# Kernel tuning notes

Hardware: AMD Instinct MI355X
Metric: run time of the kernel (lower is better)

The kernel has to match this reference:

```python
import jax, jax.numpy as jnp
import numpy as np

B, LQ, LS, S = 64, 64, 512, 512
NEG = -1e6


def mask_for_lengths(lengths, max_len, mask_right=True):
    pos = jnp.arange(max_len)
    if mask_right:
        m = pos[None, :] >= lengths[:, None]
    else:
        m = pos[None, :] < lengths[:, None]
    return jnp.where(m, jnp.float32(NEG), jnp.float32(0.0))


def setup_inputs() -> dict:
    key = jax.random.key(0)
    ks = jax.random.split(key, 12)
    f = lambda k, shp: jax.random.normal(k, shp, jnp.float32)
    sc = np.float32(1.0 / np.sqrt(S))
    return {
        "encoded_question": f(ks[0], (B, LQ, S)),
        "encoded_support": f(ks[1], (B, LS, S)),
        "question_length": jax.random.randint(ks[2], (B,), 1, LQ + 1),
        "support_length": jax.random.randint(ks[3], (B,), LS // 2, LS + 1),
        "correct_start": jax.random.randint(ks[4], (B,), 0, LS),
        "answer2question": jnp.arange(B),
        "is_eval": 1,
        "W_qa": f(ks[5], (S, 1)) * sc,
        "W_qsi": f(ks[6], (S, S)) * sc,
        "b_qsi": jnp.zeros((S,), jnp.float32),
        "W_qs": f(ks[7], (2 * S, S)) * sc,
        "W_ss": f(ks[8], (S, 1)) * sc,
        "W_qei": f(ks[9], (S, S)) * sc,
        "b_qei": jnp.zeros((S,), jnp.float32),
        "W_qe": f(ks[10], (3 * S, S)) * sc,
        "W_es": f(ks[11], (S, 1)) * sc,
    }


def reference(encoded_question, encoded_support, question_length, support_length,
              correct_start, answer2question, is_eval,
              W_qa, W_qsi, b_qsi, W_qs, W_ss, W_qei, b_qei, W_qe, W_es):
    # question attention pooling
    att = jnp.einsum('bqd,do->bq', encoded_question, W_qa)
    att = att + mask_for_lengths(question_length, LQ)
    w = jax.nn.softmax(att, axis=1)                                   # [B,LQ]
    q_state = jnp.einsum('bqd,bq->bd', encoded_question, w)           # [B,S]

    # start scoring
    start_input = jnp.concatenate(
        [q_state[:, None, :] * encoded_support, encoded_support], axis=2)  # [B,LS,2S]
    q_start_inter = q_state @ W_qsi + b_qsi                           # [B,S]
    q_start_state = start_input @ W_qs + q_start_inter[:, None, :]    # [B,LS,S]
    support_mask = mask_for_lengths(support_length, LS)
    start_scores = jnp.einsum('bld,do->bl', jax.nn.relu(q_start_state), W_ss)
    start_scores = start_scores + support_mask                        # [B,LS]
    predicted_start_pointer = jnp.argmax(start_scores, axis=1)        # [B]

    # eval path: start_pointer = predicted argmax
    start_pointer = predicted_start_pointer
    u_s = jnp.take_along_axis(encoded_support,
                              start_pointer[:, None, None], axis=1)[:, 0, :]  # [B,S]

    # end scoring
    end_input = jnp.concatenate(
        [encoded_support * u_s[:, None, :], start_input], axis=2)     # [B,LS,3S]
    q_end_inter = q_state @ W_qei + b_qei
    q_end_state = end_input @ W_qe + q_end_inter[:, None, :]          # [B,LS,S]
    end_scores = jnp.einsum('bld,do->bl', jax.nn.relu(q_end_state), W_es)
    end_scores = end_scores + support_mask
    # eval: mask positions left of start_pointer
    end_scores = end_scores + mask_for_lengths(start_pointer, LS, mask_right=False)
    predicted_end_pointer = jnp.argmax(end_scores, axis=1)

    return (start_scores, end_scores, predicted_start_pointer, predicted_end_pointer)
```

## Files before the change

### kernel.cpp

```cpp
#include <hip/hip_runtime.h>
#include <math.h>

constexpr int B_  = 64;
constexpr int LQ_ = 64;
constexpr int LS_ = 512;
constexpr int S_  = 512;
#define NEGV (-1e6f)
#define MARGIN 0.0625f

typedef __attribute__((ext_vector_type(8))) short bf16x8;
typedef __attribute__((ext_vector_type(4))) float f32x4;

__device__ inline unsigned short f2bf_rn(float x) {
    unsigned u = __builtin_bit_cast(unsigned, x);
    unsigned r = (u + 0x7FFFu + ((u >> 16) & 1u)) >> 16;
    return (unsigned short)r;
}

__global__ __launch_bounds__(512)
void prep_support_kernel(const float* __restrict__ support, short* __restrict__ Aprep)
{
    int bid = blockIdx.x;
    int b = bid >> 3, rg = bid & 7;
    int t = threadIdx.x;
    int r  = t & 63;
    int cg = t >> 6;
    int row  = rg * 64 + r;
    int rc   = row >> 8;
    int rowp = row & 255;
    const float* src = support + ((size_t)(b * LS_ + row)) * S_;

    #pragma unroll
    for (int ii = 0; ii < 2; ++ii) {
        int i = cg * 2 + ii;
        #pragma unroll
        for (int kc = 0; kc < 4; ++kc) {
            int d0 = i * 32 + kc * 8;
            float4 f0 = *(const float4*)(src + d0);
            float4 f1 = *(const float4*)(src + d0 + 4);
            uint4 H;
            H.x = f2bf_rn(f0.x) | ((unsigned)f2bf_rn(f0.y) << 16);
            H.y = f2bf_rn(f0.z) | ((unsigned)f2bf_rn(f0.w) << 16);
            H.z = f2bf_rn(f1.x) | ((unsigned)f2bf_rn(f1.y) << 16);
            H.w = f2bf_rn(f1.z) | ((unsigned)f2bf_rn(f1.w) << 16);
            size_t off = ((size_t)(b * 2 + rc) * 16 + i) * 8192 + kc * 2048 + rowp * 8;
            *(uint4*)&Aprep[off] = H;
        }
    }
}

__global__ __launch_bounds__(256)
void qpool_kernel(const float* __restrict__ eq, const int* __restrict__ qlen,
                  const float* __restrict__ W_qa, float* __restrict__ q_state)
{
    int b = blockIdx.x;
    int t = threadIdx.x;
    int wave = t >> 6, lane = t & 63;
    __shared__ float att[LQ_];
    __shared__ float wsm[LQ_];
    const float* eqb = eq + (size_t)b * LQ_ * S_;

    for (int k = 0; k < 16; ++k) {
        int q = wave + 4 * k;
        const float* row = eqb + q * S_;
        float s = 0.f;
        #pragma unroll
        for (int j = 0; j < S_ / 64; ++j)
            s = fmaf(row[lane + 64 * j], W_qa[lane + 64 * j], s);
        #pragma unroll
        for (int off = 32; off >= 1; off >>= 1)
            s += __shfl_xor(s, off);
        if (lane == 0) att[q] = s;
    }
    __syncthreads();

    if (wave == 0) {
        int L = qlen[b];
        float v = att[lane] + ((lane < L) ? 0.f : NEGV);
        float m = v;
        #pragma unroll
        for (int off = 32; off >= 1; off >>= 1)
            m = fmaxf(m, __shfl_xor(m, off));
        float e = expf(v - m);
        float sum = e;
        #pragma unroll
        for (int off = 32; off >= 1; off >>= 1)
            sum += __shfl_xor(sum, off);
        wsm[lane] = e / sum;
    }
    __syncthreads();

    for (int d = t; d < S_; d += 256) {
        float acc = 0.f;
        #pragma unroll 8
        for (int q = 0; q < LQ_; ++q)
            acc = fmaf(wsm[q], eqb[q * S_ + d], acc);
        q_state[b * S_ + d] = acc;
    }
}

__global__ __launch_bounds__(512)
void inter_kernel(const float* __restrict__ q_state,
                  const float* __restrict__ W_qsi, const float* __restrict__ b_qsi,
                  const float* __restrict__ W_qei, const float* __restrict__ b_qei,
                  float* __restrict__ qsi, float* __restrict__ qei)
{
    int b = blockIdx.x;
    const float* W  = blockIdx.y ? W_qei : W_qsi;
    const float* bi = blockIdx.y ? b_qei : b_qsi;
    float*       o  = blockIdx.y ? qei   : qsi;
    int t = threadIdx.x, lane = t & 63, w = t >> 6;
    __shared__ float qs[S_];
    __shared__ float red[8][S_];
    qs[t] = q_state[b * S_ + t];
    __syncthreads();

    float z[8];
    #pragma unroll
    for (int k = 0; k < 8; ++k) z[k] = 0.f;
    const int d0 = w * 64;
    #pragma unroll 4
    for (int dd = 0; dd < 64; ++dd) {
        int d = d0 + dd;
        float q = qs[d];
        const float* row = W + (size_t)d * S_ + lane;
        #pragma unroll
        for (int k = 0; k < 8; ++k)
            z[k] = fmaf(q, row[k * 64], z[k]);
    }
    #pragma unroll
    for (int k = 0; k < 8; ++k) red[w][k * 64 + lane] = z[k];
    __syncthreads();
    float acc = bi[t];
    #pragma unroll
    for (int ww = 0; ww < 8; ++ww) acc += red[ww][t];
    o[b * S_ + t] = acc;
}

template <int NT>
__global__ __launch_bounds__(512)
void prep_kernel(const float* __restrict__ W, const float* __restrict__ q_state,
                 const float* __restrict__ u_s, short* __restrict__ Wc)
{
    int bid = blockIdx.x;
    int i = bid >> 6, b = bid & 63;
    int col = threadIdx.x;
    int cc = col >> 8, colp = col & 255;
    __shared__ float scq[32], scu[32];
    if (col < 32) scq[col] = q_state[b * S_ + i * 32 + col];
    if (NT == 3 && col >= 32 && col < 64) scu[col - 32] = u_s[b * S_ + i * 32 + col - 32];
    __syncthreads();

    unsigned short h[32];
    #pragma unroll
    for (int d = 0; d < 32; ++d) {
        int D = i * 32 + d;
        float v;
        if (NT == 2)
            v = fmaf(scq[d], W[(size_t)D * S_ + col], W[(size_t)(S_ + D) * S_ + col]);
        else
            v = fmaf(scu[d], W[(size_t)D * S_ + col],
                fmaf(scq[d], W[(size_t)(S_ + D) * S_ + col], W[(size_t)(2 * S_ + D) * S_ + col]));
        h[d] = f2bf_rn(v);
    }
    size_t base = ((size_t)(b * 2 + cc) * 16 + i) * 8192 + (size_t)colp * 8;
    #pragma unroll
    for (int kc = 0; kc < 4; ++kc) {
        uint4 H;
        H.x = h[kc*8+0] | ((unsigned)h[kc*8+1] << 16);
        H.y = h[kc*8+2] | ((unsigned)h[kc*8+3] << 16);
        H.z = h[kc*8+4] | ((unsigned)h[kc*8+5] << 16);
        H.w = h[kc*8+6] | ((unsigned)h[kc*8+7] << 16);
        *(uint4*)&Wc[base + kc * 2048] = H;
    }
}

__global__ __launch_bounds__(512, 2)
void score_kernel(const short* __restrict__ Aprep, const short* __restrict__ Wc,
                  const float* __restrict__ inter, const float* __restrict__ Wsmall,
                  float* __restrict__ out)
{
    const int t = threadIdx.x;
    const int lane = t & 63, wid = t >> 6;
    const int wr = wid >> 2, wc = wid & 3;
    const int l15 = lane & 15, l4 = lane >> 4;

    int lid = blockIdx.x;
    int xcd = lid & 7, slot = lid >> 3;
    int b  = xcd * 8 + (slot >> 2);
    int rc = (slot >> 1) & 1;
    int cc = slot & 1;

    __shared__ __attribute__((aligned(16))) short As[2][8192];
    __shared__ __attribute__((aligned(16))) short Bs[2][8192];
    __shared__ float int_l[256], wsm_l[256];
    __shared__ float sm_red[256][4];

    if (t < 256) {
        int_l[t] = inter[b * S_ + cc * 256 + t];
        wsm_l[t] = Wsmall[cc * 256 + t];
    }

    const char* Abase = (const char*)(Aprep + ((size_t)(b * 2 + rc) * 16) * 8192);
    const char* Bbase = (const char*)(Wc    + ((size_t)(b * 2 + cc) * 16) * 8192);

    f32x4 acc[8][4];
    #pragma unroll
    for (int r = 0; r < 8; ++r)
        #pragma unroll
        for (int c = 0; c < 4; ++c)
            acc[r][c] = (f32x4){0.f, 0.f, 0.f, 0.f};

    auto stage = [&](int i, int buf) {
        const char* ga = Abase + (size_t)i * 16384 + t * 16;
        const char* gb = Bbase + (size_t)i * 16384 + t * 16;
        char* la = (char*)As[buf] + t * 16;
        char* lb = (char*)Bs[buf] + t * 16;
        __builtin_amdgcn_global_load_lds(
            (const __attribute__((address_space(1))) void*)ga,
            (__attribute__((address_space(3))) void*)la, 16, 0, 0);
        __builtin_amdgcn_global_load_lds(
            (const __attribute__((address_space(1))) void*)(ga + 8192),
            (__attribute__((address_space(3))) void*)(la + 8192), 16, 0, 0);
        __builtin_amdgcn_global_load_lds(
            (const __attribute__((address_space(1))) void*)gb,
            (__attribute__((address_space(3))) void*)lb, 16, 0, 0);
        __builtin_amdgcn_global_load_lds(
            (const __attribute__((address_space(1))) void*)(gb + 8192),
            (__attribute__((address_space(3))) void*)(lb + 8192), 16, 0, 0);
    };

    stage(0, 0);

    for (int i = 0; i < 16; ++i) {
        const int buf = i & 1;
        if (i + 1 < 16) {
            stage(i + 1, buf ^ 1);
            asm volatile("s_waitcnt vmcnt(4)" ::: "memory");
        } else {
            asm volatile("s_waitcnt vmcnt(0)" ::: "memory");
        }
        __builtin_amdgcn_s_barrier();

        bf16x8 ah[8];
        #pragma unroll
        for (int r = 0; r < 8; ++r) {
            int rowp = wr * 128 + r * 16 + l15;
            ah[r] = *(const bf16x8*)&As[buf][l4 * 2048 + rowp * 8];
        }
        #pragma unroll
        for (int c = 0; c < 4; ++c) {
            int colp = wc * 64 + c * 16 + l15;
            bf16x8 bh = *(const bf16x8*)&Bs[buf][l4 * 2048 + colp * 8];
            #pragma unroll
            for (int r = 0; r < 8; ++r)
                acc[r][c] = __builtin_amdgcn_mfma_f32_16x16x32_bf16(ah[r], bh, acc[r][c], 0, 0, 0);
        }
        asm volatile("s_waitcnt lgkmcnt(0)" ::: "memory");
        __builtin_amdgcn_s_barrier();
    }

    #pragma unroll
    for (int r = 0; r < 8; ++r) {
        #pragma unroll
        for (int jj = 0; jj < 4; ++jj) {
            float pr = 0.f;
            #pragma unroll
            for (int c = 0; c < 4; ++c) {
                int colp = wc * 64 + c * 16 + l15;
                float v = acc[r][c][jj] + int_l[colp];
                v = fmaxf(v, 0.f);
                pr = fmaf(v, wsm_l[colp], pr);
            }
            pr += __shfl_xor(pr, 1);
            pr += __shfl_xor(pr, 2);
            pr += __shfl_xor(pr, 4);
            pr += __shfl_xor(pr, 8);
            if (l15 == 0) sm_red[wr * 128 + r * 16 + l4 * 4 + jj][wc] = pr;
        }
    }
    __syncthreads();
    if (t < 256) {
        int l = rc * 256 + t;
        float s = sm_red[t][0] + sm_red[t][1] + sm_red[t][2] + sm_red[t][3];
        out[((size_t)cc * B_ * LS_) + b * LS_ + l] = s;
    }
}

__global__ __launch_bounds__(256)
void combine_kernel(const float* __restrict__ part0, const float* __restrict__ part1,
                    const int* __restrict__ slen, const int* __restrict__ sp,
                    int endflag, float* __restrict__ out)
{
    int g = blockIdx.x * 256 + threadIdx.x;
    int b = g >> 9, l = g & 511;
    float s = part0[g] + part1[g];
    if (l >= slen[b]) s += NEGV;
    if (endflag && l < sp[b]) s += NEGV;
    out[g] = s;
}

__device__ inline int select_cands(const float* s_l, int t, int lane, int w,
                                   float* wred, int* wcnt, int* cand)
{
    float v = s_l[t];
    #pragma unroll
    for (int off = 32; off >= 1; off >>= 1)
        v = fmaxf(v, __shfl_xor(v, off));
    if (lane == 0) wred[w] = v;
    __syncthreads();
    float m = wred[0];
    #pragma unroll
    for (int k = 1; k < 8; ++k) m = fmaxf(m, wred[k]);
    float th = m - MARGIN;
    bool flag = s_l[t] >= th;
    unsigned long long bal = __ballot(flag);
    int rank = __popcll(bal & ((1ull << lane) - 1ull));
    if (lane == 0) wcnt[w] = (int)__popcll(bal);
    __syncthreads();
    int off = 0, total = 0;
    #pragma unroll
    for (int k = 0; k < 8; ++k) { if (k < w) off += wcnt[k]; total += wcnt[k]; }
    if (flag) { int pos = off + rank; if (pos < 8) cand[pos] = t; }
    __syncthreads();
    return total < 8 ? total : 8;
}

template <bool END>
__global__ __launch_bounds__(512)
void rescue_kernel(const float* __restrict__ support, const float* __restrict__ q_state,
                   const float* __restrict__ u_s, const float* __restrict__ Wbig,
                   const float* __restrict__ inter, const float* __restrict__ Wsmall,
                   const float* __restrict__ scores, float* __restrict__ part)
{
    int bid = blockIdx.x;
    int b = bid >> 2, chunk = bid & 3;
    int t = threadIdx.x, lane = t & 63, w = t >> 6;
    __shared__ float s_l[S_], qs_l[S_], us_l[S_];
    __shared__ float arow[8][S_];
    __shared__ float red[8][8][128];
    __shared__ float wred[8];
    __shared__ int wcnt[8], cand[8];

    s_l[t]  = scores[b * S_ + t];
    qs_l[t] = q_state[b * S_ + t];
    if (END) us_l[t] = u_s[b * S_ + t];
    #pragma unroll
    for (int c = 0; c < 8; ++c) arow[c][t] = 0.f;
    __syncthreads();

    int cnt = select_cands(s_l, t, lane, w, wred, wcnt, cand);

    for (int c = 0; c < cnt; ++c)
        arow[c][t] = support[((size_t)(b * LS_ + cand[c])) * S_ + t];
    __syncthreads();

    float z0[8], z1[8];
    #pragma unroll
    for (int c = 0; c < 8; ++c) { z0[c] = 0.f; z1[c] = 0.f; }

    const int d0 = w * 64;
    const int s0 = chunk * 128 + lane, s1 = s0 + 64;
    const float* W1 = Wbig;
    const float* W2 = Wbig + (size_t)S_ * S_;
    const float* W3 = Wbig + (size_t)2 * S_ * S_;

    #pragma unroll 4
    for (int dd = 0; dd < 64; ++dd) {
        int d = d0 + dd;
        float r1a = W1[(size_t)d * S_ + s0], r1b = W1[(size_t)d * S_ + s1];
        float r2a = W2[(size_t)d * S_ + s0], r2b = W2[(size_t)d * S_ + s1];
        float r3a = 0.f, r3b = 0.f;
        if (END) { r3a = W3[(size_t)d * S_ + s0]; r3b = W3[(size_t)d * S_ + s1]; }
        float q = qs_l[d];
        float u = END ? us_l[d] : 0.f;
        #pragma unroll
        for (int c = 0; c < 8; ++c) {
            float a = arow[c][d];
            if (END) {
                float ua = u * a, qa = q * a;
                z0[c] = fmaf(ua, r1a, fmaf(qa, r2a, fmaf(a, r3a, z0[c])));
                z1[c] = fmaf(ua, r1b, fmaf(qa, r2b, fmaf(a, r3b, z1[c])));
            } else {
                float qa = q * a;
                z0[c] = fmaf(qa, r1a, fmaf(a, r2a, z0[c]));
                z1[c] = fmaf(qa, r1b, fmaf(a, r2b, z1[c]));
            }
        }
    }
    #pragma unroll
    for (int c = 0; c < 8; ++c) {
        red[w][c][lane]      = z0[c];
        red[w][c][64 + lane] = z1[c];
    }
    __syncthreads();

    {
        float a0 = 0.f, a1 = 0.f;
        #pragma unroll
        for (int ww = 0; ww < 8; ++ww) {
            a0 += red[ww][w][lane];
            a1 += red[ww][w][64 + lane];
        }
        float v0 = fmaxf(a0 + inter[b * S_ + s0], 0.f) * Wsmall[s0];
        float v1 = fmaxf(a1 + inter[b * S_ + s1], 0.f) * Wsmall[s1];
        float p = v0 + v1;
        #pragma unroll
        for (int off = 32; off >= 1; off >>= 1)
            p += __shfl_xor(p, off);
        if (lane == 0 && w < cnt) part[((size_t)b * 8 + w) * 4 + chunk] = p;
    }
}

template <bool END>
__global__ __launch_bounds__(512)
void finalize_kernel(const float* __restrict__ scores, const float* __restrict__ part,
                     const float* __restrict__ support, int* __restrict__ sp_ws,
                     float* __restrict__ pred, float* __restrict__ us_out)
{
    int b = blockIdx.x;
    int t = threadIdx.x, lane = t & 63, w = t >> 6;
    __shared__ float s_l[S_];
    __shared__ float wred[8];
    __shared__ int wcnt[8], cand[8];
    __shared__ int best_sh;

    s_l[t] = scores[b * S_ + t];
    __syncthreads();
    int cnt = select_cands(s_l, t, lane, w, wred, wcnt, cand);

    if (t == 0) {
        float bv = -INFINITY;
        int bi = cand[0];
        for (int c = 0; c < cnt; ++c) {
            const float* pp = part + ((size_t)b * 8 + c) * 4;
            float e = ((pp[0] + pp[1]) + pp[2]) + pp[3];
            if (e > bv) { bv = e; bi = cand[c]; }
        }
        best_sh = bi;
        pred[b] = (float)bi;
        if (!END) sp_ws[b] = bi;
    }
    __syncthreads();
    if (!END)
        us_out[b * S_ + t] = support[((size_t)(b * LS_ + best_sh)) * S_ + t];
}

extern "C" void kernel_launch(void* const* d_in, const int* in_sizes, int n_in,
                              void* d_out, int out_size, void* d_ws, size_t ws_size,
                              hipStream_t stream)
{
    const float* eq    = (const float*)d_in[0];
    const float* es    = (const float*)d_in[1];
    const int*   qlen  = (const int*)d_in[2];
    const int*   slen  = (const int*)d_in[3];
    const float* W_qa  = (const float*)d_in[7];
    const float* W_qsi = (const float*)d_in[8];
    const float* b_qsi = (const float*)d_in[9];
    const float* W_qs  = (const float*)d_in[10];
    const float* W_ss  = (const float*)d_in[11];
    const float* W_qei = (const float*)d_in[12];
    const float* b_qei = (const float*)d_in[13];
    const float* W_qe  = (const float*)d_in[14];
    const float* W_es  = (const float*)d_in[15];

    float* out          = (float*)d_out;
    float* start_scores = out;
    float* end_scores   = out + B_ * LS_;
    float* pred_start   = out + 2 * B_ * LS_;
    float* pred_end     = out + 2 * B_ * LS_ + B_;

    float* ws      = (float*)d_ws;
    float* q_state = ws;
    float* qsi     = ws + B_ * S_;
    float* qei     = ws + 2 * B_ * S_;
    float* u_s     = ws + 3 * B_ * S_;
    float* part    = ws + 4 * B_ * S_;
    int*   sp_ws   = (int*)(ws + 4 * B_ * S_ + 2048);
    float* scpart  = ws + 4 * B_ * S_ + 4096;
    short* Wc      = (short*)(scpart + 2 * B_ * LS_);
    short* Aprep   = Wc + (size_t)B_ * 2 * 16 * 8192;

    prep_support_kernel<<<512, 512, 0, stream>>>(es, Aprep);
    qpool_kernel<<<B_, 256, 0, stream>>>(eq, qlen, W_qa, q_state);
    inter_kernel<<<dim3(B_, 2), 512, 0, stream>>>(q_state, W_qsi, b_qsi, W_qei, b_qei, qsi, qei);

    prep_kernel<2><<<1024, 512, 0, stream>>>(W_qs, q_state, nullptr, Wc);
    score_kernel<<<256, 512, 0, stream>>>(Aprep, Wc, qsi, W_ss, scpart);
    combine_kernel<<<B_ * LS_ / 256, 256, 0, stream>>>(scpart, scpart + B_ * LS_,
                                                       slen, sp_ws, 0, start_scores);
    rescue_kernel<false><<<256, 512, 0, stream>>>(es, q_state, nullptr, W_qs, qsi, W_ss,
                                                  start_scores, part);
    finalize_kernel<false><<<B_, 512, 0, stream>>>(start_scores, part, es, sp_ws, pred_start, u_s);

    prep_kernel<3><<<1024, 512, 0, stream>>>(W_qe, q_state, u_s, Wc);
    score_kernel<<<256, 512, 0, stream>>>(Aprep, Wc, qei, W_es, scpart);
    combine_kernel<<<B_ * LS_ / 256, 256, 0, stream>>>(scpart, scpart + B_ * LS_,
                                                       slen, sp_ws, 1, end_scores);
    rescue_kernel<true><<<256, 512, 0, stream>>>(es, q_state, u_s, W_qe, qei, W_es,
                                                 end_scores, part);
    finalize_kernel<true><<<B_, 512, 0, stream>>>(end_scores, part, es, nullptr, pred_end, nullptr);
}
```

Measured before the change: 190.4 us.

## Retile score GEMM to full columns, fuse combine and rescue-finalize kernels

```diff
diff --git a/kernel.cpp b/kernel.cpp
--- a/kernel.cpp
+++ b/kernel.cpp
@@ -26,7 +26,7 @@
     int r  = t & 63;
     int cg = t >> 6;
     int row  = rg * 64 + r;
-    int rc   = row >> 8;
+    int rc2  = row >> 8;
     int rowp = row & 255;
     const float* src = support + ((size_t)(b * LS_ + row)) * S_;
 
@@ -43,7 +43,7 @@
             H.y = f2bf_rn(f0.z) | ((unsigned)f2bf_rn(f0.w) << 16);
             H.z = f2bf_rn(f1.x) | ((unsigned)f2bf_rn(f1.y) << 16);
             H.w = f2bf_rn(f1.z) | ((unsigned)f2bf_rn(f1.w) << 16);
-            size_t off = ((size_t)(b * 2 + rc) * 16 + i) * 8192 + kc * 2048 + rowp * 8;
+            size_t off = ((size_t)(b * 2 + rc2) * 16 + i) * 8192 + kc * 2048 + rowp * 8;
             *(uint4*)&Aprep[off] = H;
         }
     }
@@ -145,7 +145,6 @@
     int bid = blockIdx.x;
     int i = bid >> 6, b = bid & 63;
     int col = threadIdx.x;
-    int cc = col >> 8, colp = col & 255;
     __shared__ float scq[32], scu[32];
     if (col < 32) scq[col] = q_state[b * S_ + i * 32 + col];
     if (NT == 3 && col >= 32 && col < 64) scu[col - 32] = u_s[b * S_ + i * 32 + col - 32];
@@ -163,7 +162,7 @@
                 fmaf(scq[d], W[(size_t)(S_ + D) * S_ + col], W[(size_t)(2 * S_ + D) * S_ + col]));
         h[d] = f2bf_rn(v);
     }
-    size_t base = ((size_t)(b * 2 + cc) * 16 + i) * 8192 + (size_t)colp * 8;
+    size_t base = ((size_t)b * 16 + i) * 16384 + (size_t)col * 8;
     #pragma unroll
     for (int kc = 0; kc < 4; ++kc) {
         uint4 H;
@@ -171,13 +170,15 @@
         H.y = h[kc*8+2] | ((unsigned)h[kc*8+3] << 16);
         H.z = h[kc*8+4] | ((unsigned)h[kc*8+5] << 16);
         H.w = h[kc*8+6] | ((unsigned)h[kc*8+7] << 16);
-        *(uint4*)&Wc[base + kc * 2048] = H;
-    }
-}
-
+        *(uint4*)&Wc[base + kc * 4096] = H;
+    }
+}
+
+template <bool END>
 __global__ __launch_bounds__(512, 2)
 void score_kernel(const short* __restrict__ Aprep, const short* __restrict__ Wc,
                   const float* __restrict__ inter, const float* __restrict__ Wsmall,
+                  const int* __restrict__ slen, const int* __restrict__ sp,
                   float* __restrict__ out)
 {
     const int t = threadIdx.x;
@@ -188,46 +189,42 @@
     int lid = blockIdx.x;
     int xcd = lid & 7, slot = lid >> 3;
     int b  = xcd * 8 + (slot >> 2);
-    int rc = (slot >> 1) & 1;
-    int cc = slot & 1;
-
-    __shared__ __attribute__((aligned(16))) short As[2][8192];
-    __shared__ __attribute__((aligned(16))) short Bs[2][8192];
-    __shared__ float int_l[256], wsm_l[256];
-    __shared__ float sm_red[256][4];
-
-    if (t < 256) {
-        int_l[t] = inter[b * S_ + cc * 256 + t];
-        wsm_l[t] = Wsmall[cc * 256 + t];
-    }
-
-    const char* Abase = (const char*)(Aprep + ((size_t)(b * 2 + rc) * 16) * 8192);
-    const char* Bbase = (const char*)(Wc    + ((size_t)(b * 2 + cc) * 16) * 8192);
-
-    f32x4 acc[8][4];
-    #pragma unroll
-    for (int r = 0; r < 8; ++r)
-        #pragma unroll
-        for (int c = 0; c < 4; ++c)
+    int rc = slot & 3;
+    int rc2 = rc >> 1, hh = rc & 1;
+
+    __shared__ __attribute__((aligned(16))) short As[2][4096];
+    __shared__ __attribute__((aligned(16))) short Bs[2][16384];
+    __shared__ float int_l[S_], wsm_l[S_];
+    __shared__ float sm_red[128][4];
+
+    int_l[t] = inter[b * S_ + t];
+    wsm_l[t] = Wsmall[t];
+
+    const char* Abase = (const char*)(Aprep + ((size_t)(b * 2 + rc2) * 16) * 8192);
+    const char* Bbase = (const char*)(Wc    + ((size_t)b * 16) * 16384);
+
+    f32x4 acc[4][8];
+    #pragma unroll
+    for (int r = 0; r < 4; ++r)
+        #pragma unroll
+        for (int c = 0; c < 8; ++c)
             acc[r][c] = (f32x4){0.f, 0.f, 0.f, 0.f};
 
+    const int akc = t >> 7, ar = t & 127;
+
     auto stage = [&](int i, int buf) {
-        const char* ga = Abase + (size_t)i * 16384 + t * 16;
-        const char* gb = Bbase + (size_t)i * 16384 + t * 16;
+        const char* ga = Abase + (size_t)i * 16384 + akc * 4096 + hh * 2048 + ar * 16;
         char* la = (char*)As[buf] + t * 16;
-        char* lb = (char*)Bs[buf] + t * 16;
         __builtin_amdgcn_global_load_lds(
             (const __attribute__((address_space(1))) void*)ga,
             (__attribute__((address_space(3))) void*)la, 16, 0, 0);
-        __builtin_amdgcn_global_load_lds(
-            (const __attribute__((address_space(1))) void*)(ga + 8192),
-            (__attribute__((address_space(3))) void*)(la + 8192), 16, 0, 0);
-        __builtin_amdgcn_global_load_lds(
-            (const __attribute__((address_space(1))) void*)gb,
-            (__attribute__((address_space(3))) void*)lb, 16, 0, 0);
-        __builtin_amdgcn_global_load_lds(
-            (const __attribute__((address_space(1))) void*)(gb + 8192),
-            (__attribute__((address_space(3))) void*)(lb + 8192), 16, 0, 0);
+        const char* gb = Bbase + (size_t)i * 32768 + t * 16;
+        char* lb = (char*)Bs[buf] + t * 16;
+        #pragma unroll
+        for (int q = 0; q < 4; ++q)
+            __builtin_amdgcn_global_load_lds(
+                (const __attribute__((address_space(1))) void*)(gb + q * 8192),
+                (__attribute__((address_space(3))) void*)(lb + q * 8192), 16, 0, 0);
     };
 
     stage(0, 0);
@@ -236,24 +233,24 @@
         const int buf = i & 1;
         if (i + 1 < 16) {
             stage(i + 1, buf ^ 1);
-            asm volatile("s_waitcnt vmcnt(4)" ::: "memory");
+            asm volatile("s_waitcnt vmcnt(5)" ::: "memory");
         } else {
             asm volatile("s_waitcnt vmcnt(0)" ::: "memory");
         }
         __builtin_amdgcn_s_barrier();
 
-        bf16x8 ah[8];
-        #pragma unroll
-        for (int r = 0; r < 8; ++r) {
-            int rowp = wr * 128 + r * 16 + l15;
-            ah[r] = *(const bf16x8*)&As[buf][l4 * 2048 + rowp * 8];
-        }
-        #pragma unroll
-        for (int c = 0; c < 4; ++c) {
-            int colp = wc * 64 + c * 16 + l15;
-            bf16x8 bh = *(const bf16x8*)&Bs[buf][l4 * 2048 + colp * 8];
-            #pragma unroll
-            for (int r = 0; r < 8; ++r)
+        bf16x8 ah[4];
+        #pragma unroll
+        for (int r = 0; r < 4; ++r) {
+            int rowp = wr * 64 + r * 16 + l15;
+            ah[r] = *(const bf16x8*)&As[buf][l4 * 1024 + rowp * 8];
+        }
+        #pragma unroll
+        for (int c = 0; c < 8; ++c) {
+            int col = wc * 128 + c * 16 + l15;
+            bf16x8 bh = *(const bf16x8*)&Bs[buf][l4 * 4096 + col * 8];
+            #pragma unroll
+            for (int r = 0; r < 4; ++r)
                 acc[r][c] = __builtin_amdgcn_mfma_f32_16x16x32_bf16(ah[r], bh, acc[r][c], 0, 0, 0);
         }
         asm volatile("s_waitcnt lgkmcnt(0)" ::: "memory");
@@ -261,43 +258,32 @@
     }
 
     #pragma unroll
-    for (int r = 0; r < 8; ++r) {
+    for (int r = 0; r < 4; ++r) {
         #pragma unroll
         for (int jj = 0; jj < 4; ++jj) {
             float pr = 0.f;
             #pragma unroll
-            for (int c = 0; c < 4; ++c) {
-                int colp = wc * 64 + c * 16 + l15;
-                float v = acc[r][c][jj] + int_l[colp];
+            for (int c = 0; c < 8; ++c) {
+                int col = wc * 128 + c * 16 + l15;
+                float v = acc[r][c][jj] + int_l[col];
                 v = fmaxf(v, 0.f);
-                pr = fmaf(v, wsm_l[colp], pr);
+                pr = fmaf(v, wsm_l[col], pr);
             }
             pr += __shfl_xor(pr, 1);
             pr += __shfl_xor(pr, 2);
             pr += __shfl_xor(pr, 4);
             pr += __shfl_xor(pr, 8);
-            if (l15 == 0) sm_red[wr * 128 + r * 16 + l4 * 4 + jj][wc] = pr;
-        }
-    }
-    __syncthreads();
-    if (t < 256) {
-        int l = rc * 256 + t;
+            if (l15 == 0) sm_red[wr * 64 + r * 16 + l4 * 4 + jj][wc] = pr;
+        }
+    }
+    __syncthreads();
+    if (t < 128) {
+        int l = rc * 128 + t;
         float s = sm_red[t][0] + sm_red[t][1] + sm_red[t][2] + sm_red[t][3];
-        out[((size_t)cc * B_ * LS_) + b * LS_ + l] = s;
-    }
-}
-
-__global__ __launch_bounds__(256)
-void combine_kernel(const float* __restrict__ part0, const float* __restrict__ part1,
-                    const int* __restrict__ slen, const int* __restrict__ sp,
-                    int endflag, float* __restrict__ out)
-{
-    int g = blockIdx.x * 256 + threadIdx.x;
-    int b = g >> 9, l = g & 511;
-    float s = part0[g] + part1[g];
-    if (l >= slen[b]) s += NEGV;
-    if (endflag && l < sp[b]) s += NEGV;
-    out[g] = s;
+        if (l >= slen[b]) s += NEGV;
+        if (END) { if (l < sp[b]) s += NEGV; }
+        out[b * LS_ + l] = s;
+    }
 }
 
 __device__ inline int select_cands(const float* s_l, int t, int lane, int w,
@@ -328,23 +314,28 @@
 
 template <bool END>
 __global__ __launch_bounds__(512)
-void rescue_kernel(const float* __restrict__ support, const float* __restrict__ q_state,
-                   const float* __restrict__ u_s, const float* __restrict__ Wbig,
-                   const float* __restrict__ inter, const float* __restrict__ Wsmall,
-                   const float* __restrict__ scores, float* __restrict__ part)
-{
-    int bid = blockIdx.x;
-    int b = bid >> 2, chunk = bid & 3;
+void rescue_fin_kernel(const float* __restrict__ support, const float* __restrict__ q_state,
+                       const float* __restrict__ u_s_in, const float* __restrict__ Wbig,
+                       const float* __restrict__ inter, const float* __restrict__ Wsmall,
+                       const float* __restrict__ scores,
+                       int* __restrict__ sp_ws, float* __restrict__ pred,
+                       float* __restrict__ us_out)
+{
+    int b = blockIdx.x;
     int t = threadIdx.x, lane = t & 63, w = t >> 6;
-    __shared__ float s_l[S_], qs_l[S_], us_l[S_];
+    __shared__ float s_l[S_], qs_l[S_], us_l[S_], int_l[S_], wsm_l[S_];
     __shared__ float arow[8][S_];
-    __shared__ float red[8][8][128];
+    __shared__ float red[8][4][S_];
     __shared__ float wred[8];
     __shared__ int wcnt[8], cand[8];
-
-    s_l[t]  = scores[b * S_ + t];
-    qs_l[t] = q_state[b * S_ + t];
-    if (END) us_l[t] = u_s[b * S_ + t];
+    __shared__ float exact_v[8];
+    __shared__ int best_sh;
+
+    s_l[t]   = scores[b * S_ + t];
+    qs_l[t]  = q_state[b * S_ + t];
+    int_l[t] = inter[b * S_ + t];
+    wsm_l[t] = Wsmall[t];
+    if (END) us_l[t] = u_s_in[b * S_ + t];
     #pragma unroll
     for (int c = 0; c < 8; ++c) arow[c][t] = 0.f;
     __syncthreads();
@@ -355,86 +346,78 @@
         arow[c][t] = support[((size_t)(b * LS_ + cand[c])) * S_ + t];
     __syncthreads();
 
-    float z0[8], z1[8];
-    #pragma unroll
-    for (int c = 0; c < 8; ++c) { z0[c] = 0.f; z1[c] = 0.f; }
-
-    const int d0 = w * 64;
-    const int s0 = chunk * 128 + lane, s1 = s0 + 64;
     const float* W1 = Wbig;
     const float* W2 = Wbig + (size_t)S_ * S_;
     const float* W3 = Wbig + (size_t)2 * S_ * S_;
-
-    #pragma unroll 4
-    for (int dd = 0; dd < 64; ++dd) {
-        int d = d0 + dd;
-        float r1a = W1[(size_t)d * S_ + s0], r1b = W1[(size_t)d * S_ + s1];
-        float r2a = W2[(size_t)d * S_ + s0], r2b = W2[(size_t)d * S_ + s1];
-        float r3a = 0.f, r3b = 0.f;
-        if (END) { r3a = W3[(size_t)d * S_ + s0]; r3b = W3[(size_t)d * S_ + s1]; }
-        float q = qs_l[d];
-        float u = END ? us_l[d] : 0.f;
-        #pragma unroll
-        for (int c = 0; c < 8; ++c) {
-            float a = arow[c][d];
-            if (END) {
-                float ua = u * a, qa = q * a;
-                z0[c] = fmaf(ua, r1a, fmaf(qa, r2a, fmaf(a, r3a, z0[c])));
-                z1[c] = fmaf(ua, r1b, fmaf(qa, r2b, fmaf(a, r3b, z1[c])));
-            } else {
-                float qa = q * a;
-                z0[c] = fmaf(qa, r1a, fmaf(a, r2a, z0[c]));
-                z1[c] = fmaf(qa, r1b, fmaf(a, r2b, z1[c]));
+    const int d0 = w * 64;
+
+    for (int g = 0; g * 4 < cnt; ++g) {
+        float z[4][8];
+        #pragma unroll
+        for (int cc = 0; cc < 4; ++cc)
+            #pragma unroll
+            for (int j = 0; j < 8; ++j) z[cc][j] = 0.f;
+
+        #pragma unroll 2
+        for (int dd = 0; dd < 64; ++dd) {
+            int d = d0 + dd;
+            float q = qs_l[d];
+            float u = END ? us_l[d] : 0.f;
+            float a[4], qa[4], ua[4];
+            #pragma unroll
+            for (int cc = 0; cc < 4; ++cc) {
+                a[cc]  = arow[g * 4 + cc][d];
+                qa[cc] = q * a[cc];
+                if (END) ua[cc] = u * a[cc];
             }
-        }
-    }
-    #pragma unroll
-    for (int c = 0; c < 8; ++c) {
-        red[w][c][lane]      = z0[c];
-        red[w][c][64 + lane] = z1[c];
-    }
-    __syncthreads();
-
-    {
-        float a0 = 0.f, a1 = 0.f;
-        #pragma unroll
-        for (int ww = 0; ww < 8; ++ww) {
-            a0 += red[ww][w][lane];
-            a1 += red[ww][w][64 + lane];
-        }
-        float v0 = fmaxf(a0 + inter[b * S_ + s0], 0.f) * Wsmall[s0];
-        float v1 = fmaxf(a1 + inter[b * S_ + s1], 0.f) * Wsmall[s1];
-        float p = v0 + v1;
-        #pragma unroll
-        for (int off = 32; off >= 1; off >>= 1)
-            p += __shfl_xor(p, off);
-        if (lane == 0 && w < cnt) part[((size_t)b * 8 + w) * 4 + chunk] = p;
-    }
-}
-
-template <bool END>
-__global__ __launch_bounds__(512)
-void finalize_kernel(const float* __restrict__ scores, const float* __restrict__ part,
-                     const float* __restrict__ support, int* __restrict__ sp_ws,
-                     float* __restrict__ pred, float* __restrict__ us_out)
-{
-    int b = blockIdx.x;
-    int t = threadIdx.x, lane = t & 63, w = t >> 6;
-    __shared__ float s_l[S_];
-    __shared__ float wred[8];
-    __shared__ int wcnt[8], cand[8];
-    __shared__ int best_sh;
-
-    s_l[t] = scores[b * S_ + t];
-    __syncthreads();
-    int cnt = select_cands(s_l, t, lane, w, wred, wcnt, cand);
+            #pragma unroll
+            for (int j = 0; j < 8; ++j) {
+                int s = lane + 64 * j;
+                float w1 = W1[(size_t)d * S_ + s];
+                float w2 = W2[(size_t)d * S_ + s];
+                if (END) {
+                    float w3 = W3[(size_t)d * S_ + s];
+                    #pragma unroll
+                    for (int cc = 0; cc < 4; ++cc)
+                        z[cc][j] = fmaf(ua[cc], w1, fmaf(qa[cc], w2, fmaf(a[cc], w3, z[cc][j])));
+                } else {
+                    #pragma unroll
+                    for (int cc = 0; cc < 4; ++cc)
+                        z[cc][j] = fmaf(qa[cc], w1, fmaf(a[cc], w2, z[cc][j]));
+                }
+            }
+        }
+        #pragma unroll
+        for (int cc = 0; cc < 4; ++cc)
+            #pragma unroll
+            for (int j = 0; j < 8; ++j)
+                red[w][cc][lane + 64 * j] = z[cc][j];
+        __syncthreads();
+
+        for (int cc = 0; cc < 4; ++cc) {
+            float v = 0.f;
+            #pragma unroll
+            for (int ww = 0; ww < 8; ++ww) v += red[ww][cc][t];
+            float p = fmaxf(v + int_l[t], 0.f) * wsm_l[t];
+            #pragma unroll
+            for (int off = 32; off >= 1; off >>= 1)
+                p += __shfl_xor(p, off);
+            if (lane == 0) wred[w] = p;
+            __syncthreads();
+            if (t == 0) {
+                float e = ((wred[0] + wred[1]) + (wred[2] + wred[3])) +
+                          ((wred[4] + wred[5]) + (wred[6] + wred[7]));
+                exact_v[g * 4 + cc] = e;
+            }
+            __syncthreads();
+        }
+    }
 
     if (t == 0) {
         float bv = -INFINITY;
         int bi = cand[0];
         for (int c = 0; c < cnt; ++c) {
-            const float* pp = part + ((size_t)b * 8 + c) * 4;
-            float e = ((pp[0] + pp[1]) + pp[2]) + pp[3];
+            float e = exact_v[c];
             if (e > bv) { bv = e; bi = cand[c]; }
         }
         best_sh = bi;
@@ -475,29 +458,21 @@
     float* qsi     = ws + B_ * S_;
     float* qei     = ws + 2 * B_ * S_;
     float* u_s     = ws + 3 * B_ * S_;
-    float* part    = ws + 4 * B_ * S_;
-    int*   sp_ws   = (int*)(ws + 4 * B_ * S_ + 2048);
-    float* scpart  = ws + 4 * B_ * S_ + 4096;
-    short* Wc      = (short*)(scpart + 2 * B_ * LS_);
-    short* Aprep   = Wc + (size_t)B_ * 2 * 16 * 8192;
+    int*   sp_ws   = (int*)(ws + 4 * B_ * S_);
+    short* Wc      = (short*)(ws + 4 * B_ * S_ + 64);
+    short* Aprep   = Wc + (size_t)B_ * 16 * 16384;
 
     prep_support_kernel<<<512, 512, 0, stream>>>(es, Aprep);
     qpool_kernel<<<B_, 256, 0, stream>>>(eq, qlen, W_qa, q_state);
     inter_kernel<<<dim3(B_, 2), 512, 0, stream>>>(q_state, W_qsi, b_qsi, W_qei, b_qei, qsi, qei);
 
     prep_kernel<2><<<1024, 512, 0, stream>>>(W_qs, q_state, nullptr, Wc);
-    score_kernel<<<256, 512, 0, stream>>>(Aprep, Wc, qsi, W_ss, scpart);
-    combine_kernel<<<B_ * LS_ / 256, 256, 0, stream>>>(scpart, scpart + B_ * LS_,
-                                                       slen, sp_ws, 0, start_scores);
-    rescue_kernel<false><<<256, 512, 0, stream>>>(es, q_state, nullptr, W_qs, qsi, W_ss,
-                                                  start_scores, part);
-    finalize_kernel<false><<<B_, 512, 0, stream>>>(start_scores, part, es, sp_ws, pred_start, u_s);
+    score_kernel<false><<<256, 512, 0, stream>>>(Aprep, Wc, qsi, W_ss, slen, nullptr, start_scores);
+    rescue_fin_kernel<false><<<B_, 512, 0, stream>>>(es, q_state, nullptr, W_qs, qsi, W_ss,
+                                                     start_scores, sp_ws, pred_start, u_s);
 
     prep_kernel<3><<<1024, 512, 0, stream>>>(W_qe, q_state, u_s, Wc);
-    score_kernel<<<256, 512, 0, stream>>>(Aprep, Wc, qei, W_es, scpart);
-    combine_kernel<<<B_ * LS_ / 256, 256, 0, stream>>>(scpart, scpart + B_ * LS_,
-                                                       slen, sp_ws, 1, end_scores);
-    rescue_kernel<true><<<256, 512, 0, stream>>>(es, q_state, u_s, W_qe, qei, W_es,
-                                                 end_scores, part);
-    finalize_kernel<true><<<B_, 512, 0, stream>>>(end_scores, part, es, nullptr, pred_end, nullptr);
-}
+    score_kernel<true><<<256, 512, 0, stream>>>(Aprep, Wc, qei, W_es, slen, sp_ws, end_scores);
+    rescue_fin_kernel<true><<<B_, 512, 0, stream>>>(es, q_state, u_s, W_qe, qei, W_es,
+                                                    end_scores, nullptr, pred_end, nullptr);
+}
```

After: 187.4 us. No clear change (-1.5%).
